# Optimization experiments

Measured on AMD Instinct MI355X. Metric: run time of the kernel, lower is better.

The kernel has to match this reference:

```python
import jax, jax.numpy as jnp
import numpy as np

N_SRC = 50000   # source nodes in the block
N_DST = 50000   # destination nodes
E = 800000      # edges (avg in-degree 16, every dst has >=1 edge)
D = 256         # hidden_dim
V = 50000       # vocab_size
C = 104         # n_classes (POJ-104)


def setup_inputs() -> dict:
    key = jax.random.key(0)
    k1, k2, k3, k4, k5, k6 = jax.random.split(key, 6)
    token_id = jax.random.randint(k1, (N_SRC,), 0, V, dtype=jnp.int32)
    src_idx = jax.random.randint(k2, (E,), 0, N_SRC, dtype=jnp.int32)
    # every dst node gets at least one in-edge (DGL raises on 0-in-degree),
    # remaining edges land on random dst nodes; sorted so edges are grouped by dst
    extra = jax.random.randint(k3, (E - N_DST,), 0, N_DST, dtype=jnp.int32)
    dst_idx = jnp.sort(jnp.concatenate([jnp.arange(N_DST, dtype=jnp.int32), extra]))
    emb = jax.random.normal(k4, (V, D), dtype=jnp.float32)  # nn.Embedding default N(0,1)
    W = jax.random.normal(k5, (D, D), dtype=jnp.float32) / jnp.sqrt(D)
    b = jnp.zeros((D,), dtype=jnp.float32)
    Wc = jax.random.normal(k6, (C, D), dtype=jnp.float32) / jnp.sqrt(D)
    bc = jnp.zeros((C,), dtype=jnp.float32)
    return {"emb": emb, "W": W, "b": b, "Wc": Wc, "bc": bc,
            "token_id": token_id, "src_idx": src_idx, "dst_idx": dst_idx}


def reference(emb, W, b, Wc, bc, token_id, src_idx, dst_idx):
    # embedding gather for source nodes (first_layer branch)
    feat_src = emb[token_id]                  # [N_SRC, D]
    # message: copy_u -> mailbox messages per edge
    msgs = feat_src[src_idx]                  # [E, D]
    # per-dst segment stats (dst_idx is sorted / grouped by dst)
    deg = jax.ops.segment_sum(jnp.ones((E,), dtype=jnp.int32), dst_idx,
                              num_segments=N_DST)            # [N_DST]
    sum_all = jax.ops.segment_sum(msgs, dst_idx, num_segments=N_DST)  # [N_DST, D]
    # DGL mailbox reducer: last message in the segment is the 'current input',
    # the rest are children summed through CodeRNNCell: x = cur + relu(W @ sum_children + b)
    last_idx = jnp.cumsum(deg) - 1            # index of last edge per dst segment
    last_msg = msgs[last_idx]                 # [N_DST, D]
    child_sum = sum_all - last_msg            # sum of msgs excluding the last one
    rnn_out = last_msg + jax.nn.relu(child_sum @ W.T + b)
    # length == 1 segments bypass the RNN cell entirely: ft = the single message
    ft = jnp.where((deg == 1)[:, None], last_msg, rnn_out)   # [N_DST, D]
    # final classifier
    return ft @ Wc.T + bc                     # [N_DST, C]
```

## Files before the change

kernel.cpp:

```cpp
#include <hip/hip_runtime.h>
#include <hip/hip_bf16.h>

#define DD 256
#define CC 104

typedef __bf16 bf16x8 __attribute__((ext_vector_type(8)));
typedef float  f32x4  __attribute__((ext_vector_type(4)));

__device__ inline unsigned short f2bu(float f) {
    __hip_bfloat16 h = __float2bfloat16(f);
    return *reinterpret_cast<unsigned short*>(&h);
}

__global__ void prep_kernel(const int* __restrict__ token_id,
                            const int* __restrict__ src_idx,
                            const int* __restrict__ dst_idx,
                            int* __restrict__ seg_start,
                            int* __restrict__ seg_end,
                            int* __restrict__ edge_tok,
                            int E)
{
    int e = blockIdx.x * blockDim.x + threadIdx.x;
    if (e >= E) return;
    int d = dst_idx[e];
    edge_tok[e] = token_id[src_idx[e]];
    if (e == 0 || dst_idx[e - 1] != d) seg_start[d] = e;
    if (e == E - 1 || dst_idx[e + 1] != d) seg_end[d] = e + 1;
}

__global__ void convert_kernel(const float* __restrict__ emb,
                               const float* __restrict__ W,
                               const float* __restrict__ Wc,
                               __hip_bfloat16* __restrict__ embb,
                               __hip_bfloat16* __restrict__ Wb,
                               __hip_bfloat16* __restrict__ Wcb,
                               int nE4)
{
    const int nW4  = DD * DD / 4;
    const int nWc4 = 128 * DD / 4;
    int i = blockIdx.x * blockDim.x + threadIdx.x;
    float4 v;
    __hip_bfloat16* dst;
    if (i < nE4) {
        v = ((const float4*)emb)[i];
        dst = embb + (size_t)i * 4;
    } else if (i < nE4 + nW4) {
        int j = i - nE4;
        v = ((const float4*)W)[j];
        dst = Wb + (size_t)j * 4;
    } else if (i < nE4 + nW4 + nWc4) {
        int j = i - nE4 - nW4;
        v = (j < CC * DD / 4) ? ((const float4*)Wc)[j]
                              : make_float4(0.f, 0.f, 0.f, 0.f);
        dst = Wcb + (size_t)j * 4;
    } else return;
    ushort4 o;
    o.x = f2bu(v.x); o.y = f2bu(v.y); o.z = f2bu(v.z); o.w = f2bu(v.w);
    *(ushort4*)dst = o;
}

__global__ void seg_sum_kernel(const __hip_bfloat16* __restrict__ embb,
                               const int* __restrict__ edge_tok,
                               const int* __restrict__ seg_start,
                               const int* __restrict__ seg_end,
                               __hip_bfloat16* __restrict__ childb,
                               int n_dst)
{
    int w = (blockIdx.x * blockDim.x + threadIdx.x) >> 6;
    int lane = threadIdx.x & 63;
    if (w >= n_dst) return;
    int h   = lane >> 5;
    int l32 = lane & 31;
    int s = seg_start[w];
    int e = seg_end[w] - 1;
    float acc[8] = {0.f,0.f,0.f,0.f,0.f,0.f,0.f,0.f};

    auto accum = [&](int tok) {
        uint4 u = *(const uint4*)(embb + (size_t)tok * DD + l32 * 8);
        const unsigned* ud = (const unsigned*)&u;
#pragma unroll
        for (int d = 0; d < 4; ++d) {
            acc[2*d]   += __uint_as_float(ud[d] << 16);
            acc[2*d+1] += __uint_as_float(ud[d] & 0xffff0000u);
        }
    };

    int i = s + h;
    for (; i + 2 < e; i += 4) {
        int t0 = edge_tok[i];
        int t1 = edge_tok[i + 2];
        uint4 u0 = *(const uint4*)(embb + (size_t)t0 * DD + l32 * 8);
        uint4 u1 = *(const uint4*)(embb + (size_t)t1 * DD + l32 * 8);
        const unsigned* a0 = (const unsigned*)&u0;
        const unsigned* a1 = (const unsigned*)&u1;
#pragma unroll
        for (int d = 0; d < 4; ++d) {
            acc[2*d]   += __uint_as_float(a0[d] << 16) + __uint_as_float(a1[d] << 16);
            acc[2*d+1] += __uint_as_float(a0[d] & 0xffff0000u) + __uint_as_float(a1[d] & 0xffff0000u);
        }
    }
    if (i < e) accum(edge_tok[i]);

#pragma unroll
    for (int j = 0; j < 8; ++j) acc[j] += __shfl_xor(acc[j], 32, 64);

    if (h == 0) {
        uint4 o;
        unsigned* od = (unsigned*)&o;
#pragma unroll
        for (int d = 0; d < 4; ++d)
            od[d] = (unsigned)f2bu(acc[2*d]) | ((unsigned)f2bu(acc[2*d+1]) << 16);
        *(uint4*)(childb + (size_t)w * DD + l32 * 8) = o;
    }
}

__global__ __launch_bounds__(256, 2) void rnn_mfma(
    __hip_bfloat16* childft,
    const __hip_bfloat16* __restrict__ Wb,
    const float* __restrict__ bvec,
    const __hip_bfloat16* __restrict__ embb,
    const int* __restrict__ seg_start,
    const int* __restrict__ seg_end,
    const int* __restrict__ edge_tok,
    int M)
{
    extern __shared__ char smem[];
    __hip_bfloat16* lds = (__hip_bfloat16*)smem;
    const int t    = threadIdx.x;
    const int lane = t & 63;
    const int wid  = t >> 6;
    const int quad = lane >> 4;
    const int l16  = lane & 15;
    const int m0   = blockIdx.x * 128 + wid * 32;

    f32x4 acc[2][16];
#pragma unroll
    for (int mt = 0; mt < 2; ++mt)
#pragma unroll
        for (int nt = 0; nt < 16; ++nt) acc[mt][nt] = (f32x4){0.f,0.f,0.f,0.f};

    const __hip_bfloat16* arow0 = childft + (size_t)min(m0 + l16, M-1) * DD + quad * 8;
    const __hip_bfloat16* arow1 = childft + (size_t)min(m0 + 16 + l16, M-1) * DD + quad * 8;

    for (int phase = 0; phase < 2; ++phase) {
        bf16x8 a0[4], a1[4];
#pragma unroll
        for (int k0l = 0; k0l < 4; ++k0l) {
            int k0 = phase * 128 + k0l * 32;
            a0[k0l] = *(const bf16x8*)(arow0 + k0);
            a1[k0l] = *(const bf16x8*)(arow1 + k0);
        }
        if (phase) __syncthreads();
#pragma unroll 4
        for (int it = 0; it < 16; ++it) {
            int idx = it * 256 + t;
            int g = idx >> 6, s = idx & 63;
            int nt = g & 15, k0l = g >> 4;
            int row = nt * 16 + (s & 15);
            int col = phase * 128 + k0l * 32 + (s >> 4) * 8;
            *(bf16x8*)(lds + g * 512 + s * 8) =
                *(const bf16x8*)(Wb + (size_t)row * DD + col);
        }
        __syncthreads();
#pragma unroll
        for (int k0l = 0; k0l < 4; ++k0l) {
#pragma unroll
            for (int nt = 0; nt < 16; ++nt) {
                bf16x8 b = *(const bf16x8*)(lds + (k0l * 16 + nt) * 512 + lane * 8);
                acc[0][nt] = __builtin_amdgcn_mfma_f32_16x16x32_bf16(a0[k0l], b, acc[0][nt], 0, 0, 0);
                acc[1][nt] = __builtin_amdgcn_mfma_f32_16x16x32_bf16(a1[k0l], b, acc[1][nt], 0, 0, 0);
            }
        }
    }

    float bias[16];
#pragma unroll
    for (int nt = 0; nt < 16; ++nt) bias[nt] = bvec[nt * 16 + l16];

#pragma unroll
    for (int mt = 0; mt < 2; ++mt) {
#pragma unroll
        for (int r = 0; r < 4; ++r) {
            int m = m0 + mt * 16 + quad * 4 + r;
            if (m < M) {
                int le = seg_end[m];
                bool multi = (le - seg_start[m]) > 1;
                int tok = edge_tok[le - 1];
                const __hip_bfloat16* lrow = embb + (size_t)tok * DD;
#pragma unroll
                for (int nt = 0; nt < 16; ++nt) {
                    int c = nt * 16 + l16;
                    float last = __bfloat162float(lrow[c]);
                    float v = multi ? fmaxf(acc[mt][nt][r] + bias[nt], 0.f) : 0.f;
                    childft[(size_t)m * DD + c] = __float2bfloat16(last + v);
                }
            }
        }
    }
}

__global__ __launch_bounds__(256, 2) void cls_mfma(
    const __hip_bfloat16* __restrict__ ftb,
    const __hip_bfloat16* __restrict__ Wcb,
    const float* __restrict__ bc,
    float* __restrict__ out,
    int M)
{
    extern __shared__ char smem[];
    __hip_bfloat16* lds = (__hip_bfloat16*)smem;
    const int t    = threadIdx.x;
    const int lane = t & 63;
    const int wid  = t >> 6;
    const int quad = lane >> 4;
    const int l16  = lane & 15;
    const int m0   = blockIdx.x * 128 + wid * 32;

    f32x4 acc[2][8];
#pragma unroll
    for (int mt = 0; mt < 2; ++mt)
#pragma unroll
        for (int nt = 0; nt < 8; ++nt) acc[mt][nt] = (f32x4){0.f,0.f,0.f,0.f};

    const __hip_bfloat16* arow0 = ftb + (size_t)min(m0 + l16, M-1) * DD + quad * 8;
    const __hip_bfloat16* arow1 = ftb + (size_t)min(m0 + 16 + l16, M-1) * DD + quad * 8;

    bf16x8 a0[8], a1[8];
#pragma unroll
    for (int k0t = 0; k0t < 8; ++k0t) {
        a0[k0t] = *(const bf16x8*)(arow0 + k0t * 32);
        a1[k0t] = *(const bf16x8*)(arow1 + k0t * 32);
    }

#pragma unroll 4
    for (int it = 0; it < 16; ++it) {
        int idx = it * 256 + t;
        int g = idx >> 6, s = idx & 63;
        int nt = g & 7, k0t = g >> 3;
        int row = nt * 16 + (s & 15);
        int col = k0t * 32 + (s >> 4) * 8;
        *(bf16x8*)(lds + g * 512 + s * 8) =
            *(const bf16x8*)(Wcb + (size_t)row * DD + col);
    }
    __syncthreads();

#pragma unroll
    for (int k0t = 0; k0t < 8; ++k0t) {
#pragma unroll
        for (int nt = 0; nt < 8; ++nt) {
            bf16x8 b = *(const bf16x8*)(lds + (k0t * 8 + nt) * 512 + lane * 8);
            acc[0][nt] = __builtin_amdgcn_mfma_f32_16x16x32_bf16(a0[k0t], b, acc[0][nt], 0, 0, 0);
            acc[1][nt] = __builtin_amdgcn_mfma_f32_16x16x32_bf16(a1[k0t], b, acc[1][nt], 0, 0, 0);
        }
    }

    float bias[8];
#pragma unroll
    for (int nt = 0; nt < 8; ++nt) {
        int c = nt * 16 + l16;
        bias[nt] = (c < CC) ? bc[c] : 0.f;
    }

#pragma unroll
    for (int mt = 0; mt < 2; ++mt) {
#pragma unroll
        for (int r = 0; r < 4; ++r) {
            int m = m0 + mt * 16 + quad * 4 + r;
            if (m < M) {
#pragma unroll
                for (int nt = 0; nt < 8; ++nt) {
                    int c = nt * 16 + l16;
                    if (c < CC)
                        out[(size_t)m * CC + c] = acc[mt][nt][r] + bias[nt];
                }
            }
        }
    }
}

extern "C" void kernel_launch(void* const* d_in, const int* in_sizes, int n_in,
                              void* d_out, int out_size, void* d_ws, size_t ws_size,
                              hipStream_t stream)
{
    const float* emb      = (const float*)d_in[0];
    const float* W        = (const float*)d_in[1];
    const float* bvec     = (const float*)d_in[2];
    const float* Wc       = (const float*)d_in[3];
    const float* bc       = (const float*)d_in[4];
    const int*   token_id = (const int*)d_in[5];
    const int*   src_idx  = (const int*)d_in[6];
    const int*   dst_idx  = (const int*)d_in[7];
    float*       out      = (float*)d_out;

    const int E     = in_sizes[6];
    const int Vemb  = in_sizes[0] / DD;
    const int n_dst = out_size / CC;
    (void)n_in; (void)ws_size;

    char* ws = (char*)d_ws;
    size_t off = 0;
    auto alloc = [&](size_t bytes) {
        void* p = ws + off;
        off = (off + bytes + 255) & ~(size_t)255;
        return p;
    };
    int* seg_start = (int*)alloc((size_t)n_dst * sizeof(int));
    int* seg_end   = (int*)alloc((size_t)n_dst * sizeof(int));
    int* edge_tok  = (int*)alloc((size_t)E * sizeof(int));
    __hip_bfloat16* childb = (__hip_bfloat16*)alloc((size_t)n_dst * DD * 2);
    __hip_bfloat16* embb   = (__hip_bfloat16*)alloc((size_t)Vemb * DD * 2);
    __hip_bfloat16* Wb     = (__hip_bfloat16*)alloc((size_t)DD * DD * 2);
    __hip_bfloat16* Wcb    = (__hip_bfloat16*)alloc((size_t)128 * DD * 2);

    const int nE4 = Vemb * (DD / 4);
    const int cvt_total = nE4 + DD * DD / 4 + 128 * DD / 4;
    const int gemm_blocks = (n_dst + 127) / 128;

    prep_kernel<<<(E + 255) / 256, 256, 0, stream>>>(
        token_id, src_idx, dst_idx, seg_start, seg_end, edge_tok, E);
    convert_kernel<<<(cvt_total + 255) / 256, 256, 0, stream>>>(
        emb, W, Wc, embb, Wb, Wcb, nE4);
    seg_sum_kernel<<<(n_dst + 3) / 4, 256, 0, stream>>>(
        embb, edge_tok, seg_start, seg_end, childb, n_dst);
    rnn_mfma<<<gemm_blocks, 256, 65536, stream>>>(
        childb, Wb, bvec, embb, seg_start, seg_end, edge_tok, n_dst);
    cls_mfma<<<gemm_blocks, 256, 65536, stream>>>(
        childb, Wcb, bc, out, n_dst);
}
```

Measured before the change: 222.0 us.

## Fuse RNN cell GEMM and classifier GEMM into one kernel via LDS staging

Merges the RNN-cell GEMM and the classifier GEMM into one kernel. The RNN output is staged in padded LDS and combined with the last-message embedding in registers, then fed straight into the classifier MFMA, so the bf16 ft tensor never round-trips through global memory. Tiles shrink to 64 rows per block with one 16-row tile per wave, weights are streamed through a smaller LDS buffer in K chunks, and occupancy is raised to 3 blocks per CU. The cost is that each block reloads both weight matrices with more barriers, and MFMA reuse of each B fragment drops from two row tiles to one.

```diff
diff --git a/kernel.cpp b/kernel.cpp
--- a/kernel.cpp
+++ b/kernel.cpp
@@ -11,6 +11,7 @@
     __hip_bfloat16 h = __float2bfloat16(f);
     return *reinterpret_cast<unsigned short*>(&h);
 }
+__device__ inline float b2f(__hip_bfloat16 h) { return __bfloat162float(h); }
 
 __global__ void prep_kernel(const int* __restrict__ token_id,
                             const int* __restrict__ src_idx,
@@ -114,14 +115,18 @@
     }
 }
 
-__global__ __launch_bounds__(256, 2) void rnn_mfma(
-    __hip_bfloat16* childft,
+#define FT_STRIDE 264
+__global__ __launch_bounds__(256, 3) void rnn_cls_mfma(
+    const __hip_bfloat16* __restrict__ childb,
     const __hip_bfloat16* __restrict__ Wb,
     const float* __restrict__ bvec,
+    const __hip_bfloat16* __restrict__ Wcb,
+    const float* __restrict__ bc,
     const __hip_bfloat16* __restrict__ embb,
     const int* __restrict__ seg_start,
     const int* __restrict__ seg_end,
     const int* __restrict__ edge_tok,
+    float* __restrict__ out,
     int M)
 {
     extern __shared__ char smem[];
@@ -131,147 +136,124 @@
     const int wid  = t >> 6;
     const int quad = lane >> 4;
     const int l16  = lane & 15;
-    const int m0   = blockIdx.x * 128 + wid * 32;
-
-    f32x4 acc[2][16];
-#pragma unroll
-    for (int mt = 0; mt < 2; ++mt)
-#pragma unroll
-        for (int nt = 0; nt < 16; ++nt) acc[mt][nt] = (f32x4){0.f,0.f,0.f,0.f};
-
-    const __hip_bfloat16* arow0 = childft + (size_t)min(m0 + l16, M-1) * DD + quad * 8;
-    const __hip_bfloat16* arow1 = childft + (size_t)min(m0 + 16 + l16, M-1) * DD + quad * 8;
-
-    for (int phase = 0; phase < 2; ++phase) {
-        bf16x8 a0[4], a1[4];
-#pragma unroll
-        for (int k0l = 0; k0l < 4; ++k0l) {
-            int k0 = phase * 128 + k0l * 32;
-            a0[k0l] = *(const bf16x8*)(arow0 + k0);
-            a1[k0l] = *(const bf16x8*)(arow1 + k0);
-        }
-        if (phase) __syncthreads();
-#pragma unroll 4
-        for (int it = 0; it < 16; ++it) {
+    const int m0   = blockIdx.x * 64;
+    const int mw   = m0 + wid * 16;
+
+    bool multi[4];
+#pragma unroll
+    for (int r = 0; r < 4; ++r) {
+        int m = min(mw + quad * 4 + r, M - 1);
+        multi[r] = (seg_end[m] - seg_start[m]) > 1;
+    }
+    int mrow = min(mw + l16, M - 1);
+    int ltok = edge_tok[seg_end[mrow] - 1];
+
+    const __hip_bfloat16* arow = childb + (size_t)mrow * DD + quad * 8;
+    bf16x8 afrag[8];
+#pragma unroll
+    for (int k = 0; k < 8; ++k)
+        afrag[k] = *(const bf16x8*)(arow + k * 32);
+
+    float bias[16];
+#pragma unroll
+    for (int nt = 0; nt < 16; ++nt) bias[nt] = bvec[nt * 16 + l16];
+
+    f32x4 acc[16];
+#pragma unroll
+    for (int nt = 0; nt < 16; ++nt) acc[nt] = (f32x4){0.f,0.f,0.f,0.f};
+
+    for (int p = 0; p < 4; ++p) {
+        __syncthreads();
+#pragma unroll
+        for (int it = 0; it < 8; ++it) {
             int idx = it * 256 + t;
             int g = idx >> 6, s = idx & 63;
-            int nt = g & 15, k0l = g >> 4;
+            int nt = g & 15, kl = g >> 4;
             int row = nt * 16 + (s & 15);
-            int col = phase * 128 + k0l * 32 + (s >> 4) * 8;
+            int col = (p * 2 + kl) * 32 + (s >> 4) * 8;
             *(bf16x8*)(lds + g * 512 + s * 8) =
                 *(const bf16x8*)(Wb + (size_t)row * DD + col);
         }
         __syncthreads();
 #pragma unroll
-        for (int k0l = 0; k0l < 4; ++k0l) {
+        for (int kl = 0; kl < 2; ++kl) {
+            bf16x8 a = afrag[p * 2 + kl];
 #pragma unroll
             for (int nt = 0; nt < 16; ++nt) {
-                bf16x8 b = *(const bf16x8*)(lds + (k0l * 16 + nt) * 512 + lane * 8);
-                acc[0][nt] = __builtin_amdgcn_mfma_f32_16x16x32_bf16(a0[k0l], b, acc[0][nt], 0, 0, 0);
-                acc[1][nt] = __builtin_amdgcn_mfma_f32_16x16x32_bf16(a1[k0l], b, acc[1][nt], 0, 0, 0);
+                bf16x8 b = *(const bf16x8*)(lds + (kl * 16 + nt) * 512 + lane * 8);
+                acc[nt] = __builtin_amdgcn_mfma_f32_16x16x32_bf16(a, b, acc[nt], 0, 0, 0);
             }
         }
     }
 
-    float bias[16];
-#pragma unroll
-    for (int nt = 0; nt < 16; ++nt) bias[nt] = bvec[nt * 16 + l16];
-
-#pragma unroll
-    for (int mt = 0; mt < 2; ++mt) {
+    __syncthreads();
+#pragma unroll
+    for (int nt = 0; nt < 16; ++nt) {
 #pragma unroll
         for (int r = 0; r < 4; ++r) {
-            int m = m0 + mt * 16 + quad * 4 + r;
-            if (m < M) {
-                int le = seg_end[m];
-                bool multi = (le - seg_start[m]) > 1;
-                int tok = edge_tok[le - 1];
-                const __hip_bfloat16* lrow = embb + (size_t)tok * DD;
-#pragma unroll
-                for (int nt = 0; nt < 16; ++nt) {
-                    int c = nt * 16 + l16;
-                    float last = __bfloat162float(lrow[c]);
-                    float v = multi ? fmaxf(acc[mt][nt][r] + bias[nt], 0.f) : 0.f;
-                    childft[(size_t)m * DD + c] = __float2bfloat16(last + v);
-                }
+            float v = multi[r] ? fmaxf(acc[nt][r] + bias[nt], 0.f) : 0.f;
+            lds[(wid * 16 + quad * 4 + r) * FT_STRIDE + nt * 16 + l16] =
+                __float2bfloat16(v);
+        }
+    }
+    __syncthreads();
+
+    const __hip_bfloat16* lrow = embb + (size_t)ltok * DD + quad * 8;
+    bf16x8 ftfrag[8];
+#pragma unroll
+    for (int k = 0; k < 8; ++k) {
+        bf16x8 rp = *(const bf16x8*)(lds + (wid * 16 + l16) * FT_STRIDE + k * 32 + quad * 8);
+        bf16x8 lm = *(const bf16x8*)(lrow + k * 32);
+        bf16x8 o;
+#pragma unroll
+        for (int j = 0; j < 8; ++j)
+            o[j] = (__bf16)(__bf16)((float)rp[j] + (float)lm[j]);
+        ftfrag[k] = o;
+    }
+
+    f32x4 acc2[8];
+#pragma unroll
+    for (int nt = 0; nt < 8; ++nt) acc2[nt] = (f32x4){0.f,0.f,0.f,0.f};
+
+    for (int p = 0; p < 2; ++p) {
+        __syncthreads();
+#pragma unroll
+        for (int it = 0; it < 8; ++it) {
+            int idx = it * 256 + t;
+            int g = idx >> 6, s = idx & 63;
+            int nt = g & 7, kt = g >> 3;
+            int row = nt * 16 + (s & 15);
+            int col = (p * 4 + kt) * 32 + (s >> 4) * 8;
+            *(bf16x8*)(lds + g * 512 + s * 8) =
+                *(const bf16x8*)(Wcb + (size_t)row * DD + col);
+        }
+        __syncthreads();
+#pragma unroll
+        for (int kt = 0; kt < 4; ++kt) {
+            bf16x8 a = ftfrag[p * 4 + kt];
+#pragma unroll
+            for (int nt = 0; nt < 8; ++nt) {
+                bf16x8 b = *(const bf16x8*)(lds + (kt * 8 + nt) * 512 + lane * 8);
+                acc2[nt] = __builtin_amdgcn_mfma_f32_16x16x32_bf16(a, b, acc2[nt], 0, 0, 0);
             }
         }
     }
-}
-
-__global__ __launch_bounds__(256, 2) void cls_mfma(
-    const __hip_bfloat16* __restrict__ ftb,
-    const __hip_bfloat16* __restrict__ Wcb,
-    const float* __restrict__ bc,
-    float* __restrict__ out,
-    int M)
-{
-    extern __shared__ char smem[];
-    __hip_bfloat16* lds = (__hip_bfloat16*)smem;
-    const int t    = threadIdx.x;
-    const int lane = t & 63;
-    const int wid  = t >> 6;
-    const int quad = lane >> 4;
-    const int l16  = lane & 15;
-    const int m0   = blockIdx.x * 128 + wid * 32;
-
-    f32x4 acc[2][8];
-#pragma unroll
-    for (int mt = 0; mt < 2; ++mt)
-#pragma unroll
-        for (int nt = 0; nt < 8; ++nt) acc[mt][nt] = (f32x4){0.f,0.f,0.f,0.f};
-
-    const __hip_bfloat16* arow0 = ftb + (size_t)min(m0 + l16, M-1) * DD + quad * 8;
-    const __hip_bfloat16* arow1 = ftb + (size_t)min(m0 + 16 + l16, M-1) * DD + quad * 8;
-
-    bf16x8 a0[8], a1[8];
-#pragma unroll
-    for (int k0t = 0; k0t < 8; ++k0t) {
-        a0[k0t] = *(const bf16x8*)(arow0 + k0t * 32);
-        a1[k0t] = *(const bf16x8*)(arow1 + k0t * 32);
-    }
-
-#pragma unroll 4
-    for (int it = 0; it < 16; ++it) {
-        int idx = it * 256 + t;
-        int g = idx >> 6, s = idx & 63;
-        int nt = g & 7, k0t = g >> 3;
-        int row = nt * 16 + (s & 15);
-        int col = k0t * 32 + (s >> 4) * 8;
-        *(bf16x8*)(lds + g * 512 + s * 8) =
-            *(const bf16x8*)(Wcb + (size_t)row * DD + col);
-    }
-    __syncthreads();
-
-#pragma unroll
-    for (int k0t = 0; k0t < 8; ++k0t) {
-#pragma unroll
-        for (int nt = 0; nt < 8; ++nt) {
-            bf16x8 b = *(const bf16x8*)(lds + (k0t * 8 + nt) * 512 + lane * 8);
-            acc[0][nt] = __builtin_amdgcn_mfma_f32_16x16x32_bf16(a0[k0t], b, acc[0][nt], 0, 0, 0);
-            acc[1][nt] = __builtin_amdgcn_mfma_f32_16x16x32_bf16(a1[k0t], b, acc[1][nt], 0, 0, 0);
-        }
-    }
-
-    float bias[8];
+
+    float bcv[8];
 #pragma unroll
     for (int nt = 0; nt < 8; ++nt) {
         int c = nt * 16 + l16;
-        bias[nt] = (c < CC) ? bc[c] : 0.f;
-    }
-
-#pragma unroll
-    for (int mt = 0; mt < 2; ++mt) {
-#pragma unroll
-        for (int r = 0; r < 4; ++r) {
-            int m = m0 + mt * 16 + quad * 4 + r;
-            if (m < M) {
-#pragma unroll
-                for (int nt = 0; nt < 8; ++nt) {
-                    int c = nt * 16 + l16;
-                    if (c < CC)
-                        out[(size_t)m * CC + c] = acc[mt][nt][r] + bias[nt];
-                }
+        bcv[nt] = (c < CC) ? bc[c] : 0.f;
+    }
+#pragma unroll
+    for (int r = 0; r < 4; ++r) {
+        int m = mw + quad * 4 + r;
+        if (m < M) {
+#pragma unroll
+            for (int nt = 0; nt < 8; ++nt) {
+                int c = nt * 16 + l16;
+                if (c < CC)
+                    out[(size_t)m * CC + c] = acc2[nt][r] + bcv[nt];
             }
         }
     }
@@ -313,7 +295,8 @@
 
     const int nE4 = Vemb * (DD / 4);
     const int cvt_total = nE4 + DD * DD / 4 + 128 * DD / 4;
-    const int gemm_blocks = (n_dst + 127) / 128;
+    const int fused_blocks = (n_dst + 63) / 64;
+    const int lds_bytes = 64 * FT_STRIDE * 2;
 
     prep_kernel<<<(E + 255) / 256, 256, 0, stream>>>(
         token_id, src_idx, dst_idx, seg_start, seg_end, edge_tok, E);
@@ -321,8 +304,7 @@
         emb, W, Wc, embb, Wb, Wcb, nE4);
     seg_sum_kernel<<<(n_dst + 3) / 4, 256, 0, stream>>>(
         embb, edge_tok, seg_start, seg_end, childb, n_dst);
-    rnn_mfma<<<gemm_blocks, 256, 65536, stream>>>(
-        childb, Wb, bvec, embb, seg_start, seg_end, edge_tok, n_dst);
-    cls_mfma<<<gemm_blocks, 256, 65536, stream>>>(
-        childb, Wcb, bc, out, n_dst);
-}
+    rnn_cls_mfma<<<fused_blocks, 256, lds_bytes, stream>>>(
+        childb, Wb, bvec, Wcb, bc, embb, seg_start, seg_end, edge_tok,
+        out, n_dst);
+}
```

Result: faster. 207.0 us (-6.8%).

## Merge prep/convert launches and transpose MFMA operands for vectorized epilogues

Applied to the files above, without the earlier changes.

The separate prep and conversion kernels become one launch whose block ranges pick the role, removing one kernel launch and its serialization gap. In both GEMM kernels the MFMA operand order is swapped so each lane's accumulator holds four consecutive columns of a single row. The epilogues can then load bias and last-message values as vectors and issue float4/ushort4 stores instead of scattered scalar writes. Per-row segment metadata is also loaded once up front, and the A-fragments are held in registers across both phases, which raises register pressure.

```diff
diff --git a/kernel.cpp b/kernel.cpp
--- a/kernel.cpp
+++ b/kernel.cpp
@@ -7,38 +7,42 @@
 typedef __bf16 bf16x8 __attribute__((ext_vector_type(8)));
 typedef float  f32x4  __attribute__((ext_vector_type(4)));
 
+__device__ inline float bu2f(unsigned short u) {
+    return __uint_as_float(((unsigned)u) << 16);
+}
 __device__ inline unsigned short f2bu(float f) {
     __hip_bfloat16 h = __float2bfloat16(f);
     return *reinterpret_cast<unsigned short*>(&h);
 }
 
-__global__ void prep_kernel(const int* __restrict__ token_id,
-                            const int* __restrict__ src_idx,
-                            const int* __restrict__ dst_idx,
-                            int* __restrict__ seg_start,
-                            int* __restrict__ seg_end,
-                            int* __restrict__ edge_tok,
-                            int E)
-{
-    int e = blockIdx.x * blockDim.x + threadIdx.x;
-    if (e >= E) return;
-    int d = dst_idx[e];
-    edge_tok[e] = token_id[src_idx[e]];
-    if (e == 0 || dst_idx[e - 1] != d) seg_start[d] = e;
-    if (e == E - 1 || dst_idx[e + 1] != d) seg_end[d] = e + 1;
-}
-
-__global__ void convert_kernel(const float* __restrict__ emb,
-                               const float* __restrict__ W,
-                               const float* __restrict__ Wc,
-                               __hip_bfloat16* __restrict__ embb,
-                               __hip_bfloat16* __restrict__ Wb,
-                               __hip_bfloat16* __restrict__ Wcb,
-                               int nE4)
-{
+__global__ void prep_convert_kernel(
+    const int* __restrict__ token_id,
+    const int* __restrict__ src_idx,
+    const int* __restrict__ dst_idx,
+    int* __restrict__ seg_start,
+    int* __restrict__ seg_end,
+    int* __restrict__ edge_tok,
+    int E, int prep_blocks,
+    const float* __restrict__ emb,
+    const float* __restrict__ W,
+    const float* __restrict__ Wc,
+    __hip_bfloat16* __restrict__ embb,
+    __hip_bfloat16* __restrict__ Wb,
+    __hip_bfloat16* __restrict__ Wcb,
+    int nE4)
+{
+    if ((int)blockIdx.x < prep_blocks) {
+        int e = blockIdx.x * blockDim.x + threadIdx.x;
+        if (e >= E) return;
+        int d = dst_idx[e];
+        edge_tok[e] = token_id[src_idx[e]];
+        if (e == 0 || dst_idx[e - 1] != d) seg_start[d] = e;
+        if (e == E - 1 || dst_idx[e + 1] != d) seg_end[d] = e + 1;
+        return;
+    }
     const int nW4  = DD * DD / 4;
     const int nWc4 = 128 * DD / 4;
-    int i = blockIdx.x * blockDim.x + threadIdx.x;
+    int i = (blockIdx.x - prep_blocks) * blockDim.x + threadIdx.x;
     float4 v;
     __hip_bfloat16* dst;
     if (i < nE4) {
@@ -131,7 +135,23 @@
     const int wid  = t >> 6;
     const int quad = lane >> 4;
     const int l16  = lane & 15;
-    const int m0   = blockIdx.x * 128 + wid * 32;
+    const int mw   = blockIdx.x * 128 + wid * 32;
+
+    int  mrow[2], ltok[2];
+    bool multi[2];
+    bf16x8 cfrag[2][8];
+#pragma unroll
+    for (int mt = 0; mt < 2; ++mt) {
+        mrow[mt] = min(mw + mt * 16 + l16, M - 1);
+        int ls = seg_start[mrow[mt]];
+        int le = seg_end[mrow[mt]];
+        multi[mt] = (le - ls) > 1;
+        ltok[mt]  = edge_tok[le - 1];
+        const __hip_bfloat16* arow = childft + (size_t)mrow[mt] * DD + quad * 8;
+#pragma unroll
+        for (int k0 = 0; k0 < 8; ++k0)
+            cfrag[mt][k0] = *(const bf16x8*)(arow + k0 * 32);
+    }
 
     f32x4 acc[2][16];
 #pragma unroll
@@ -139,61 +159,51 @@
 #pragma unroll
         for (int nt = 0; nt < 16; ++nt) acc[mt][nt] = (f32x4){0.f,0.f,0.f,0.f};
 
-    const __hip_bfloat16* arow0 = childft + (size_t)min(m0 + l16, M-1) * DD + quad * 8;
-    const __hip_bfloat16* arow1 = childft + (size_t)min(m0 + 16 + l16, M-1) * DD + quad * 8;
-
-    for (int phase = 0; phase < 2; ++phase) {
-        bf16x8 a0[4], a1[4];
-#pragma unroll
-        for (int k0l = 0; k0l < 4; ++k0l) {
-            int k0 = phase * 128 + k0l * 32;
-            a0[k0l] = *(const bf16x8*)(arow0 + k0);
-            a1[k0l] = *(const bf16x8*)(arow1 + k0);
-        }
-        if (phase) __syncthreads();
-#pragma unroll 4
+    for (int p = 0; p < 2; ++p) {
+        if (p) __syncthreads();
+#pragma unroll
         for (int it = 0; it < 16; ++it) {
             int idx = it * 256 + t;
             int g = idx >> 6, s = idx & 63;
-            int nt = g & 15, k0l = g >> 4;
+            int nt = g & 15, kl = g >> 4;
             int row = nt * 16 + (s & 15);
-            int col = phase * 128 + k0l * 32 + (s >> 4) * 8;
+            int col = (p * 4 + kl) * 32 + (s >> 4) * 8;
             *(bf16x8*)(lds + g * 512 + s * 8) =
                 *(const bf16x8*)(Wb + (size_t)row * DD + col);
         }
         __syncthreads();
 #pragma unroll
-        for (int k0l = 0; k0l < 4; ++k0l) {
+        for (int kl = 0; kl < 4; ++kl) {
 #pragma unroll
             for (int nt = 0; nt < 16; ++nt) {
-                bf16x8 b = *(const bf16x8*)(lds + (k0l * 16 + nt) * 512 + lane * 8);
-                acc[0][nt] = __builtin_amdgcn_mfma_f32_16x16x32_bf16(a0[k0l], b, acc[0][nt], 0, 0, 0);
-                acc[1][nt] = __builtin_amdgcn_mfma_f32_16x16x32_bf16(a1[k0l], b, acc[1][nt], 0, 0, 0);
+                bf16x8 wf = *(const bf16x8*)(lds + (kl * 16 + nt) * 512 + lane * 8);
+                acc[0][nt] = __builtin_amdgcn_mfma_f32_16x16x32_bf16(wf, cfrag[0][p*4+kl], acc[0][nt], 0, 0, 0);
+                acc[1][nt] = __builtin_amdgcn_mfma_f32_16x16x32_bf16(wf, cfrag[1][p*4+kl], acc[1][nt], 0, 0, 0);
             }
         }
     }
 
-    float bias[16];
-#pragma unroll
-    for (int nt = 0; nt < 16; ++nt) bias[nt] = bvec[nt * 16 + l16];
-
 #pragma unroll
     for (int mt = 0; mt < 2; ++mt) {
-#pragma unroll
-        for (int r = 0; r < 4; ++r) {
-            int m = m0 + mt * 16 + quad * 4 + r;
-            if (m < M) {
-                int le = seg_end[m];
-                bool multi = (le - seg_start[m]) > 1;
-                int tok = edge_tok[le - 1];
-                const __hip_bfloat16* lrow = embb + (size_t)tok * DD;
-#pragma unroll
-                for (int nt = 0; nt < 16; ++nt) {
-                    int c = nt * 16 + l16;
-                    float last = __bfloat162float(lrow[c]);
-                    float v = multi ? fmaxf(acc[mt][nt][r] + bias[nt], 0.f) : 0.f;
-                    childft[(size_t)m * DD + c] = __float2bfloat16(last + v);
-                }
+        int m = mw + mt * 16 + l16;
+        if (m < M) {
+            const __hip_bfloat16* lrow = embb + (size_t)ltok[mt] * DD;
+            bool mu = multi[mt];
+#pragma unroll
+            for (int nt = 0; nt < 16; ++nt) {
+                int c0 = nt * 16 + quad * 4;
+                float4 bia = *(const float4*)(bvec + c0);
+                ushort4 lm = *(const ushort4*)(lrow + c0);
+                ushort4 o;
+                float v0 = mu ? fmaxf(acc[mt][nt][0] + bia.x, 0.f) : 0.f;
+                float v1 = mu ? fmaxf(acc[mt][nt][1] + bia.y, 0.f) : 0.f;
+                float v2 = mu ? fmaxf(acc[mt][nt][2] + bia.z, 0.f) : 0.f;
+                float v3 = mu ? fmaxf(acc[mt][nt][3] + bia.w, 0.f) : 0.f;
+                o.x = f2bu(v0 + bu2f(lm.x));
+                o.y = f2bu(v1 + bu2f(lm.y));
+                o.z = f2bu(v2 + bu2f(lm.z));
+                o.w = f2bu(v3 + bu2f(lm.w));
+                *(ushort4*)(childft + (size_t)m * DD + c0) = o;
             }
         }
     }
@@ -213,64 +223,62 @@
     const int wid  = t >> 6;
     const int quad = lane >> 4;
     const int l16  = lane & 15;
-    const int m0   = blockIdx.x * 128 + wid * 32;
-
-    f32x4 acc[2][8];
-#pragma unroll
-    for (int mt = 0; mt < 2; ++mt)
-#pragma unroll
-        for (int nt = 0; nt < 8; ++nt) acc[mt][nt] = (f32x4){0.f,0.f,0.f,0.f};
-
-    const __hip_bfloat16* arow0 = ftb + (size_t)min(m0 + l16, M-1) * DD + quad * 8;
-    const __hip_bfloat16* arow1 = ftb + (size_t)min(m0 + 16 + l16, M-1) * DD + quad * 8;
-
-    bf16x8 a0[8], a1[8];
-#pragma unroll
-    for (int k0t = 0; k0t < 8; ++k0t) {
-        a0[k0t] = *(const bf16x8*)(arow0 + k0t * 32);
-        a1[k0t] = *(const bf16x8*)(arow1 + k0t * 32);
-    }
-
-#pragma unroll 4
+    const int mw   = blockIdx.x * 128 + wid * 32;
+
+    int mrow[2];
+    bf16x8 ffrag[2][8];
+#pragma unroll
+    for (int mt = 0; mt < 2; ++mt) {
+        mrow[mt] = min(mw + mt * 16 + l16, M - 1);
+        const __hip_bfloat16* arow = ftb + (size_t)mrow[mt] * DD + quad * 8;
+#pragma unroll
+        for (int k0 = 0; k0 < 8; ++k0)
+            ffrag[mt][k0] = *(const bf16x8*)(arow + k0 * 32);
+    }
+
+#pragma unroll
     for (int it = 0; it < 16; ++it) {
         int idx = it * 256 + t;
         int g = idx >> 6, s = idx & 63;
-        int nt = g & 7, k0t = g >> 3;
+        int nt = g & 7, k0 = g >> 3;
         int row = nt * 16 + (s & 15);
-        int col = k0t * 32 + (s >> 4) * 8;
+        int col = k0 * 32 + (s >> 4) * 8;
         *(bf16x8*)(lds + g * 512 + s * 8) =
             *(const bf16x8*)(Wcb + (size_t)row * DD + col);
     }
     __syncthreads();
 
-#pragma unroll
-    for (int k0t = 0; k0t < 8; ++k0t) {
+    f32x4 acc[2][8];
+#pragma unroll
+    for (int mt = 0; mt < 2; ++mt)
+#pragma unroll
+        for (int nt = 0; nt < 8; ++nt) acc[mt][nt] = (f32x4){0.f,0.f,0.f,0.f};
+
+#pragma unroll
+    for (int k0 = 0; k0 < 8; ++k0) {
 #pragma unroll
         for (int nt = 0; nt < 8; ++nt) {
-            bf16x8 b = *(const bf16x8*)(lds + (k0t * 8 + nt) * 512 + lane * 8);
-            acc[0][nt] = __builtin_amdgcn_mfma_f32_16x16x32_bf16(a0[k0t], b, acc[0][nt], 0, 0, 0);
-            acc[1][nt] = __builtin_amdgcn_mfma_f32_16x16x32_bf16(a1[k0t], b, acc[1][nt], 0, 0, 0);
-        }
-    }
-
-    float bias[8];
-#pragma unroll
-    for (int nt = 0; nt < 8; ++nt) {
-        int c = nt * 16 + l16;
-        bias[nt] = (c < CC) ? bc[c] : 0.f;
+            bf16x8 wf = *(const bf16x8*)(lds + (k0 * 8 + nt) * 512 + lane * 8);
+            acc[0][nt] = __builtin_amdgcn_mfma_f32_16x16x32_bf16(wf, ffrag[0][k0], acc[0][nt], 0, 0, 0);
+            acc[1][nt] = __builtin_amdgcn_mfma_f32_16x16x32_bf16(wf, ffrag[1][k0], acc[1][nt], 0, 0, 0);
+        }
     }
 
 #pragma unroll
     for (int mt = 0; mt < 2; ++mt) {
-#pragma unroll
-        for (int r = 0; r < 4; ++r) {
-            int m = m0 + mt * 16 + quad * 4 + r;
-            if (m < M) {
-#pragma unroll
-                for (int nt = 0; nt < 8; ++nt) {
-                    int c = nt * 16 + l16;
-                    if (c < CC)
-                        out[(size_t)m * CC + c] = acc[mt][nt][r] + bias[nt];
+        int m = mw + mt * 16 + l16;
+        if (m < M) {
+#pragma unroll
+            for (int nt = 0; nt < 8; ++nt) {
+                int c0 = nt * 16 + quad * 4;
+                if (c0 <= 100) {
+                    float4 bia = *(const float4*)(bc + c0);
+                    float4 o;
+                    o.x = acc[mt][nt][0] + bia.x;
+                    o.y = acc[mt][nt][1] + bia.y;
+                    o.z = acc[mt][nt][2] + bia.z;
+                    o.w = acc[mt][nt][3] + bia.w;
+                    *(float4*)(out + (size_t)m * CC + c0) = o;
                 }
             }
         }
@@ -312,13 +320,14 @@
     __hip_bfloat16* Wcb    = (__hip_bfloat16*)alloc((size_t)128 * DD * 2);
 
     const int nE4 = Vemb * (DD / 4);
-    const int cvt_total = nE4 + DD * DD / 4 + 128 * DD / 4;
+    const int cvt_total   = nE4 + DD * DD / 4 + 128 * DD / 4;
+    const int prep_blocks = (E + 255) / 256;
+    const int cvt_blocks  = (cvt_total + 255) / 256;
     const int gemm_blocks = (n_dst + 127) / 128;
 
-    prep_kernel<<<(E + 255) / 256, 256, 0, stream>>>(
-        token_id, src_idx, dst_idx, seg_start, seg_end, edge_tok, E);
-    convert_kernel<<<(cvt_total + 255) / 256, 256, 0, stream>>>(
-        emb, W, Wc, embb, Wb, Wcb, nE4);
+    prep_convert_kernel<<<prep_blocks + cvt_blocks, 256, 0, stream>>>(
+        token_id, src_idx, dst_idx, seg_start, seg_end, edge_tok, E,
+        prep_blocks, emb, W, Wc, embb, Wb, Wcb, nE4);
     seg_sum_kernel<<<(n_dst + 3) / 4, 256, 0, stream>>>(
         embb, edge_tok, seg_start, seg_end, childb, n_dst);
     rnn_mfma<<<gemm_blocks, 256, 65536, stream>>>(
```

Measured after the change: 199.7 us. 10.0% less time.
